# Performance work log

Measured on AMD Instinct MI355X. Metric: run time of the kernel, lower is better.

The kernel has to match this reference:

```python
import jax, jax.numpy as jnp
import numpy as np

# MoE_Bottleneck constants from source
E = 4   # number of experts
K = 2   # top-k routing


def setup_inputs() -> dict:
    key = jax.random.key(0)
    ks = jax.random.split(key, 10)
    B, C1, H, W = 8, 256, 64, 64
    C2 = 256
    Ch = C2 // 2  # c_ = int(c2*0.5) = 128
    x = jax.random.normal(ks[0], (B, C1, H, W), dtype=jnp.float32)
    # Conv = conv2d(no bias)+BN+SiLU; BN folded into weight scale + bias (eval mode).
    W1 = jax.random.normal(ks[1], (Ch, C1), dtype=jnp.float32) / np.sqrt(C1)
    b1 = jax.random.normal(ks[2], (Ch,), dtype=jnp.float32) * 0.1
    Wr = jax.random.normal(ks[3], (E, Ch), dtype=jnp.float32) / np.sqrt(Ch)
    br = jax.random.normal(ks[4], (E,), dtype=jnp.float32) * 0.1
    # Expert Conv(c_, c_, 3, 1): full 3x3 kernels [E, Cout, Cin, 3, 3]
    We = jax.random.normal(ks[5], (E, Ch, Ch, 3, 3), dtype=jnp.float32) / np.sqrt(Ch * 9)
    be = jax.random.normal(ks[6], (E, Ch), dtype=jnp.float32) * 0.1
    W3 = jax.random.normal(ks[7], (C2, Ch), dtype=jnp.float32) / np.sqrt(Ch)
    b3 = jax.random.normal(ks[8], (C2,), dtype=jnp.float32) * 0.1
    return {"x": x, "W1": W1, "b1": b1, "Wr": Wr, "br": br,
            "We": We, "be": be, "W3": W3, "b3": b3}


def reference(x, W1, b1, Wr, br, We, be, W3, b3):
    silu = jax.nn.silu
    # conv1: 1x1 conv + (folded BN) + SiLU
    x_in = silu(jnp.einsum('bchw,oc->bohw', x, W1) + b1[None, :, None, None])
    B, C, H, Wd = x_in.shape
    N = B * H * Wd
    xr = x_in.transpose(0, 2, 3, 1).reshape(N, C)            # [N, C] tokens
    # router: 1x1 conv -> per-pixel logits over E experts
    logits = xr @ Wr.T + br                                   # [N, E]
    probs = jax.nn.softmax(logits, axis=-1)
    topw, topi = jax.lax.top_k(probs, K)                      # [N, K]
    topw = topw / jnp.sum(topw, axis=-1, keepdims=True)       # renormalize top-k
    # dense [N, E] routing-weight matrix (indices within a row are unique)
    wmat = jnp.zeros_like(probs).at[jnp.arange(N)[:, None], topi].set(topw)
    # Experts: 3x3 conv applied to 1x1 spatial patches with pad=1 -> only the
    # center tap We[..., 1, 1] contributes (padding is zeros). Folded-BN bias + SiLU.
    Wc = We[:, :, :, 1, 1]                                    # [E, Cout, Cin]
    eout = silu(jnp.einsum('nc,eoc->neo', xr, Wc) + be[None]) # [N, E, C]
    moe = jnp.einsum('neo,ne->no', eout, wmat)                # weighted combine
    out = moe.reshape(B, H, Wd, C).transpose(0, 3, 1, 2)
    # conv3: 1x1 conv + SiLU
    y = silu(jnp.einsum('bchw,oc->bohw', out, W3) + b3[None, :, None, None])
    # shortcut=True and c1 == c2
    return y + x
```

## Files before the change

kernel.cpp:

```cpp
#include <hip/hip_runtime.h>
#include <hip/hip_bf16.h>


typedef unsigned short u16;
typedef unsigned int   u32;
typedef __attribute__((ext_vector_type(8))) short short8;
typedef __attribute__((ext_vector_type(4))) float f32x4;

#define MFMA16 __builtin_amdgcn_mfma_f32_16x16x32_bf16

__device__ __forceinline__ float silu_f(float v) { return v / (1.0f + __expf(-v)); }
__device__ __forceinline__ u16 f2bf(float f) {
    u32 u = __float_as_uint(f);
    return (u16)((u + 0x7fff + ((u >> 16) & 1)) >> 16);
}
__device__ __forceinline__ float bf2f(u16 h) { return __uint_as_float(((u32)h) << 16); }
__device__ __forceinline__ u32 pkbf(float a, float b) {
    __hip_bfloat162 h2 = __float22bfloat162_rn(make_float2(a, b));
    u32 r; __builtin_memcpy(&r, &h2, 4); return r;
}
__device__ __forceinline__ int swzkey(int row) { return (row ^ (row >> 2)) & 7; }

__global__ void prep_weights(const float* __restrict__ W1,
                             const float* __restrict__ We,
                             const float* __restrict__ W3,
                             u16* __restrict__ ws)
{
    int idx = blockIdx.x * 256 + threadIdx.x;
    if (idx < 36864) {
        int kc = idx / 9216, r = idx % 9216;
        int n = r / 72, j = r % 72;
        float v = (j < 64) ? W1[n * 256 + kc * 64 + j] : 0.0f;
        u16 h = f2bf(v);
        float lo = v - bf2f(h);
        ws[idx] = h;
        ws[36864 + idx] = f2bf(lo);
    } else if (idx < 102400) {
        int i = idx - 36864;
        int e = i >> 14, r = i & 16383;
        int o = r >> 7, rem = r & 127;
        int ps = rem >> 3, t = rem & 7;
        int gi = (ps & 8) | ((ps ^ swzkey(o)) & 7);
        int c = gi * 8 + t;
        ws[73728 + i] = f2bf(We[(size_t)(((e * 128 + o) * 128 + c) * 9) + 4]);
    } else if (idx < 135168) {
        int i = idx - 102400;
        int h = i >> 14, r = i & 16383;
        int o = r >> 7, rem = r & 127;
        int ps = rem >> 3, t = rem & 7;
        int gi = (ps & 8) | ((ps ^ swzkey(o)) & 7);
        int c = gi * 8 + t;
        ws[139264 + i] = f2bf(W3[(size_t)(h * 128 + o) * 128 + c]);
    }
}

__device__ __forceinline__ void stage_chunk(const u16* __restrict__ g, u16* l, int tid) {
#pragma unroll
    for (int i = 0; i < 8; ++i)
        __builtin_amdgcn_global_load_lds(g + (size_t)(i * 256 + tid) * 8,
                                         l + (size_t)(i * 256 + (tid & 192)) * 8, 16, 0, 0);
}
__device__ __forceinline__ void dma_u16(const u16* __restrict__ g, u16* l, int i, int tid) {
    int idx = i * 256 + tid;
    int ub  = i * 256 + (tid & 192);
    __builtin_amdgcn_global_load_lds(g + (size_t)idx * 8, l + ub * 8, 16, 0, 0);
}

__global__ __launch_bounds__(256, 2)
void fused_moe_mfma(const float* __restrict__ x,
                    const float* __restrict__ b1,
                    const float* __restrict__ Wrg,
                    const float* __restrict__ br,
                    const float* __restrict__ be,
                    const float* __restrict__ b3,
                    const u16* __restrict__ wbf,
                    float* __restrict__ out)
{
    __shared__ __align__(16) unsigned char smem[81920];
    u16*   const sWhi = (u16*)(smem);
    u16*   const sWlo = (u16*)(smem + 18432);
    u16*   const sAhi = (u16*)(smem + 36864);
    u16*   const sAlo = (u16*)(smem + 46080);
    u16*   const A2   = (u16*)(smem);
    u16*   const bufA = (u16*)(smem + 16384);
    u16*   const bufB = (u16*)(smem + 49152);
    float* const sY   = (float*)(smem + 16384);

    const int tid = threadIdx.x;
    const int l  = tid & 63;
    const int w  = tid >> 6;
    const int lr = l & 15;
    const int g  = l >> 4;
    const int lk = g * 8;
    const int mrow = 16 * w + 4 * g;
    const int arow = 16 * w + lr;
    const int akey = swzkey(arow);
    int okey[8];
#pragma unroll
    for (int f = 0; f < 8; ++f) okey[f] = swzkey(16 * f + lr);

    const int n0  = blockIdx.x << 6;
    const float* xb = x   + ((size_t)(n0 >> 12) * 256) * 4096 + (n0 & 4095);
    float*       ob = out + ((size_t)(n0 >> 12) * 256) * 4096 + (n0 & 4095);

    f32x4 acc1[8];
#pragma unroll
    for (int f = 0; f < 8; ++f) acc1[f] = (f32x4){0.f, 0.f, 0.f, 0.f};

    const int c2a = tid >> 4;
    const int c2b = 16 + c2a;
    const int m4  = (tid & 15) << 2;

#pragma unroll 1
    for (int kc = 0; kc < 4; ++kc) {
        __syncthreads();
        const float* xa0 = xb + (size_t)(kc * 64 + 2 * c2a) * 4096 + m4;
        const float* xa1 = xb + (size_t)(kc * 64 + 2 * c2b) * 4096 + m4;
        float4 fa0 = *(const float4*)xa0;
        float4 fb0 = *(const float4*)(xa0 + 4096);
        float4 fa1 = *(const float4*)xa1;
        float4 fb1 = *(const float4*)(xa1 + 4096);
#pragma unroll
        for (int i = 0; i < 5; ++i) {
            if (i * 256 + tid < 1152) {
                dma_u16(wbf + (size_t)kc * 9216,           sWhi, i, tid);
                dma_u16(wbf + (size_t)(36864 + kc * 9216), sWlo, i, tid);
            }
        }
        u32* H = (u32*)sAhi; u32* L = (u32*)sAlo;
        {
            float fav[4] = {fa0.x, fa0.y, fa0.z, fa0.w};
            float fbv[4] = {fb0.x, fb0.y, fb0.z, fb0.w};
#pragma unroll
            for (int r = 0; r < 4; ++r) {
                int ui = (m4 + r) * 36 + c2a;
                u32 hi = pkbf(fav[r], fbv[r]);
                float la = fav[r] - __uint_as_float(hi << 16);
                float lb = fbv[r] - __uint_as_float(hi & 0xffff0000u);
                H[ui] = hi; L[ui] = pkbf(la, lb);
            }
        }
        {
            float fav[4] = {fa1.x, fa1.y, fa1.z, fa1.w};
            float fbv[4] = {fb1.x, fb1.y, fb1.z, fb1.w};
#pragma unroll
            for (int r = 0; r < 4; ++r) {
                int ui = (m4 + r) * 36 + c2b;
                u32 hi = pkbf(fav[r], fbv[r]);
                float la = fav[r] - __uint_as_float(hi << 16);
                float lb = fbv[r] - __uint_as_float(hi & 0xffff0000u);
                H[ui] = hi; L[ui] = pkbf(la, lb);
            }
        }
        __syncthreads();
#pragma unroll
        for (int ks = 0; ks < 2; ++ks) {
            short8 ah = *(const short8*)&sAhi[(16 * w + lr) * 72 + ks * 32 + lk];
            short8 al = *(const short8*)&sAlo[(16 * w + lr) * 72 + ks * 32 + lk];
#pragma unroll
            for (int f = 0; f < 8; ++f) {
                int bo = (16 * f + lr) * 72 + ks * 32 + lk;
                short8 bh = *(const short8*)&sWhi[bo];
                short8 bl = *(const short8*)&sWlo[bo];
                acc1[f] = MFMA16(ah, bh, acc1[f], 0, 0, 0);
                acc1[f] = MFMA16(al, bh, acc1[f], 0, 0, 0);
                acc1[f] = MFMA16(ah, bl, acc1[f], 0, 0, 0);
                acc1[f] = MFMA16(al, bl, acc1[f], 0, 0, 0);
            }
        }
    }
    __syncthreads();

    stage_chunk(wbf + 73728,         bufA, tid);
    stage_chunk(wbf + 73728 + 16384, bufB, tid);

    float xin[8][4];
#pragma unroll
    for (int f = 0; f < 8; ++f) {
        float bias = b1[16 * f + lr];
#pragma unroll
        for (int i = 0; i < 4; ++i) xin[f][i] = silu_f(acc1[f][i] + bias);
    }
#pragma unroll
    for (int f = 0; f < 8; ++f) {
        int c = 16 * f + lr, gi = c >> 3;
#pragma unroll
        for (int i = 0; i < 4; ++i) {
            int m = mrow + i;
            int ps = (gi & 8) | ((gi ^ swzkey(m)) & 7);
            A2[m * 128 + ps * 8 + (c & 7)] = f2bf(xin[f][i]);
        }
    }

    float lg[4][4];
#pragma unroll
    for (int e = 0; e < 4; ++e)
#pragma unroll
        for (int i = 0; i < 4; ++i) lg[e][i] = 0.f;
#pragma unroll
    for (int f = 0; f < 8; ++f) {
        int c = 16 * f + lr;
        float w0 = Wrg[c], w1 = Wrg[128 + c], w2 = Wrg[256 + c], w3 = Wrg[384 + c];
#pragma unroll
        for (int i = 0; i < 4; ++i) {
            float xv = xin[f][i];
            lg[0][i] += xv * w0; lg[1][i] += xv * w1;
            lg[2][i] += xv * w2; lg[3][i] += xv * w3;
        }
    }
#pragma unroll
    for (int d = 1; d < 16; d <<= 1)
#pragma unroll
        for (int e = 0; e < 4; ++e)
#pragma unroll
            for (int i = 0; i < 4; ++i)
                lg[e][i] += __shfl_xor(lg[e][i], d, 64);

    float br0 = br[0], br1 = br[1], br2 = br[2], br3 = br[3];
    float rw[4][4];
#pragma unroll
    for (int i = 0; i < 4; ++i) {
        float le0 = lg[0][i] + br0, le1 = lg[1][i] + br1;
        float le2 = lg[2][i] + br2, le3 = lg[3][i] + br3;
        int c0 = (le1 > le0) + (le2 > le0) + (le3 > le0);
        int c1 = (le0 >= le1) + (le2 > le1) + (le3 > le1);
        int c2 = (le0 >= le2) + (le1 >= le2) + (le3 > le2);
        int c3 = (le0 >= le3) + (le1 >= le3) + (le2 >= le3);
        float m = fmaxf(fmaxf(le0, le1), fmaxf(le2, le3));
        float p0 = (c0 < 2) ? __expf(le0 - m) : 0.f;
        float p1 = (c1 < 2) ? __expf(le1 - m) : 0.f;
        float p2 = (c2 < 2) ? __expf(le2 - m) : 0.f;
        float p3 = (c3 < 2) ? __expf(le3 - m) : 0.f;
        float inv = 1.0f / (p0 + p1 + p2 + p3);
        rw[0][i] = p0 * inv; rw[1][i] = p1 * inv;
        rw[2][i] = p2 * inv; rw[3][i] = p3 * inv;
    }
    __syncthreads();

    f32x4 macc[8];
#pragma unroll
    for (int f = 0; f < 8; ++f) macc[f] = (f32x4){0.f, 0.f, 0.f, 0.f};

#pragma unroll 1
    for (int e = 0; e < 4; ++e) {
        const u16* Wb = (e & 1) ? bufB : bufA;
        f32x4 acce[8];
#pragma unroll
        for (int f = 0; f < 8; ++f) acce[f] = (f32x4){0.f, 0.f, 0.f, 0.f};
#pragma unroll
        for (int ks = 0; ks < 4; ++ks) {
            int gi = ks * 4 + g;
            int psA = (gi & 8) | ((gi ^ akey) & 7);
            short8 a = *(const short8*)&A2[arow * 128 + psA * 8];
#pragma unroll
            for (int f = 0; f < 8; ++f) {
                int psB = (gi & 8) | ((gi ^ okey[f]) & 7);
                short8 bb = *(const short8*)&Wb[(16 * f + lr) * 128 + psB * 8];
                acce[f] = MFMA16(a, bb, acce[f], 0, 0, 0);
            }
        }
#pragma unroll
        for (int f = 0; f < 8; ++f) {
            float bias = be[e * 128 + 16 * f + lr];
#pragma unroll
            for (int i = 0; i < 4; ++i)
                macc[f][i] += rw[e][i] * silu_f(acce[f][i] + bias);
        }
        __syncthreads();
        if (e < 2)      stage_chunk(wbf + 73728 + (e + 2) * 16384, (e & 1) ? bufB : bufA, tid);
        else if (e == 2) stage_chunk(wbf + 139264,                 bufA, tid);
        else              ;
    }

#pragma unroll
    for (int f = 0; f < 8; ++f) {
        int c = 16 * f + lr, gi = c >> 3;
#pragma unroll
        for (int i = 0; i < 4; ++i) {
            int m = mrow + i;
            int ps = (gi & 8) | ((gi ^ swzkey(m)) & 7);
            A2[m * 128 + ps * 8 + (c & 7)] = f2bf(macc[f][i]);
        }
    }
    __syncthreads();
    stage_chunk(wbf + 139264 + 16384, bufB, tid);

#pragma unroll 1
    for (int h = 0; h < 2; ++h) {
        const u16* Wb = h ? bufB : bufA;
        f32x4 acc3[8];
#pragma unroll
        for (int f = 0; f < 8; ++f) acc3[f] = (f32x4){0.f, 0.f, 0.f, 0.f};
#pragma unroll
        for (int ks = 0; ks < 4; ++ks) {
            int gi = ks * 4 + g;
            int psA = (gi & 8) | ((gi ^ akey) & 7);
            short8 a = *(const short8*)&A2[arow * 128 + psA * 8];
#pragma unroll
            for (int f = 0; f < 8; ++f) {
                int psB = (gi & 8) | ((gi ^ okey[f]) & 7);
                short8 bb = *(const short8*)&Wb[(16 * f + lr) * 128 + psB * 8];
                acc3[f] = MFMA16(a, bb, acc3[f], 0, 0, 0);
            }
        }
        __syncthreads();
        int mg = mrow >> 2;
#pragma unroll
        for (int f = 0; f < 8; ++f) {
            int o = 16 * f + lr;
            float bias = b3[h * 128 + o];
            float4 v;
            v.x = silu_f(acc3[f][0] + bias);
            v.y = silu_f(acc3[f][1] + bias);
            v.z = silu_f(acc3[f][2] + bias);
            v.w = silu_f(acc3[f][3] + bias);
            *(float4*)&sY[o * 64 + ((mg ^ okey[f]) << 2)] = v;
        }
        __syncthreads();
#pragma unroll
        for (int q = 0; q < 8; ++q) {
            int idx = q * 256 + tid;
            int o = idx >> 4, mq = idx & 15;
            int og = h * 128 + o;
            float4 vy = *(const float4*)&sY[o * 64 + ((mq ^ swzkey(o)) << 2)];
            size_t goff = (size_t)og * 4096 + (mq << 2);
            float4 r = *(const float4*)&xb[goff];
            vy.x += r.x; vy.y += r.y; vy.z += r.z; vy.w += r.w;
            *(float4*)&ob[goff] = vy;
        }
        if (h == 0) __syncthreads();
    }
}

extern "C" void kernel_launch(void* const* d_in, const int* in_sizes, int n_in,
                              void* d_out, int out_size, void* d_ws, size_t ws_size,
                              hipStream_t stream)
{
    const float* x  = (const float*)d_in[0];
    const float* W1 = (const float*)d_in[1];
    const float* b1 = (const float*)d_in[2];
    const float* Wr = (const float*)d_in[3];
    const float* br = (const float*)d_in[4];
    const float* We = (const float*)d_in[5];
    const float* be = (const float*)d_in[6];
    const float* W3 = (const float*)d_in[7];
    const float* b3 = (const float*)d_in[8];
    float* outp = (float*)d_out;
    u16* wbf = (u16*)d_ws;

    hipLaunchKernelGGL(prep_weights, dim3(528), dim3(256), 0, stream,
                       W1, We, W3, wbf);
    hipLaunchKernelGGL(fused_moe_mfma, dim3(512), dim3(256), 0, stream,
                       x, b1, Wr, br, be, b3, wbf, outp);
}
```

Before: 54.31 us.

## Split fused MoE kernel into three stage kernels with global intermediates

```diff
diff --git a/kernel.cpp b/kernel.cpp
--- a/kernel.cpp
+++ b/kernel.cpp
@@ -9,6 +9,13 @@
 
 #define MFMA16 __builtin_amdgcn_mfma_f32_16x16x32_bf16
 
+#define W1_OFF   0
+#define WE_OFF   65536
+#define W3_OFF   131072
+#define XIN_OFF  163840
+#define MOE_OFF  4358144
+#define RW_OFFU  8552448
+
 __device__ __forceinline__ float silu_f(float v) { return v / (1.0f + __expf(-v)); }
 __device__ __forceinline__ u16 f2bf(float f) {
     u32 u = __float_as_uint(f);
@@ -19,7 +26,8 @@
     __hip_bfloat162 h2 = __float22bfloat162_rn(make_float2(a, b));
     u32 r; __builtin_memcpy(&r, &h2, 4); return r;
 }
-__device__ __forceinline__ int swzkey(int row) { return (row ^ (row >> 2)) & 7; }
+__device__ __forceinline__ int key3(int r) { return (r ^ (r >> 2)) & 7; }
+__device__ __forceinline__ int key2(int r) { return (r ^ (r >> 2)) & 3; }
 
 __global__ void prep_weights(const float* __restrict__ W1,
                              const float* __restrict__ We,
@@ -27,141 +35,117 @@
                              u16* __restrict__ ws)
 {
     int idx = blockIdx.x * 256 + threadIdx.x;
-    if (idx < 36864) {
-        int kc = idx / 9216, r = idx % 9216;
-        int n = r / 72, j = r % 72;
-        float v = (j < 64) ? W1[n * 256 + kc * 64 + j] : 0.0f;
+    if (idx < 65536) {
+        int c4 = idx >> 14, r = idx & 16383;
+        int half = r >> 13, q = r & 8191;
+        int o = q >> 6, rem = q & 63;
+        int ps = rem >> 3, t = rem & 7;
+        int gi = (ps ^ key3(o)) & 7;
+        float v = W1[o * 256 + c4 * 64 + gi * 8 + t];
         u16 h = f2bf(v);
-        float lo = v - bf2f(h);
-        ws[idx] = h;
-        ws[36864 + idx] = f2bf(lo);
-    } else if (idx < 102400) {
-        int i = idx - 36864;
+        ws[idx] = half ? f2bf(v - bf2f(h)) : h;
+    } else if (idx < 131072) {
+        int i = idx - 65536;
         int e = i >> 14, r = i & 16383;
         int o = r >> 7, rem = r & 127;
         int ps = rem >> 3, t = rem & 7;
-        int gi = (ps & 8) | ((ps ^ swzkey(o)) & 7);
-        int c = gi * 8 + t;
-        ws[73728 + i] = f2bf(We[(size_t)(((e * 128 + o) * 128 + c) * 9) + 4]);
-    } else if (idx < 135168) {
-        int i = idx - 102400;
+        int gi = (ps & 8) | ((ps ^ key3(o)) & 7);
+        ws[idx] = f2bf(We[(size_t)(((e * 128 + o) * 128 + gi * 8 + t) * 9) + 4]);
+    } else if (idx < 163840) {
+        int i = idx - 131072;
         int h = i >> 14, r = i & 16383;
         int o = r >> 7, rem = r & 127;
         int ps = rem >> 3, t = rem & 7;
-        int gi = (ps & 8) | ((ps ^ swzkey(o)) & 7);
-        int c = gi * 8 + t;
-        ws[139264 + i] = f2bf(W3[(size_t)(h * 128 + o) * 128 + c]);
-    }
-}
-
-__device__ __forceinline__ void stage_chunk(const u16* __restrict__ g, u16* l, int tid) {
-#pragma unroll
-    for (int i = 0; i < 8; ++i)
-        __builtin_amdgcn_global_load_lds(g + (size_t)(i * 256 + tid) * 8,
-                                         l + (size_t)(i * 256 + (tid & 192)) * 8, 16, 0, 0);
-}
-__device__ __forceinline__ void dma_u16(const u16* __restrict__ g, u16* l, int i, int tid) {
-    int idx = i * 256 + tid;
-    int ub  = i * 256 + (tid & 192);
-    __builtin_amdgcn_global_load_lds(g + (size_t)idx * 8, l + ub * 8, 16, 0, 0);
-}
-
-__global__ __launch_bounds__(256, 2)
-void fused_moe_mfma(const float* __restrict__ x,
-                    const float* __restrict__ b1,
-                    const float* __restrict__ Wrg,
-                    const float* __restrict__ br,
-                    const float* __restrict__ be,
-                    const float* __restrict__ b3,
-                    const u16* __restrict__ wbf,
-                    float* __restrict__ out)
+        int gi = (ps & 8) | ((ps ^ key3(o)) & 7);
+        ws[131072 + i] = f2bf(W3[(size_t)(h * 128 + o) * 128 + gi * 8 + t]);
+    }
+}
+
+template<int ITER>
+__device__ __forceinline__ void stage512(const u16* __restrict__ g, u16* l, int tid) {
+#pragma unroll
+    for (int i = 0; i < ITER; ++i)
+        __builtin_amdgcn_global_load_lds(g + (size_t)(i * 512 + tid) * 8,
+                                         l + (size_t)(i * 512 + (tid & 448)) * 8, 16, 0, 0);
+}
+
+__global__ __launch_bounds__(512, 1)
+void k_gemm1(const float* __restrict__ x, const float* __restrict__ b1g,
+             const float* __restrict__ Wrg, const float* __restrict__ brg,
+             const u16* __restrict__ wbf, u16* __restrict__ xinG,
+             float* __restrict__ rwG)
 {
-    __shared__ __align__(16) unsigned char smem[81920];
-    u16*   const sWhi = (u16*)(smem);
-    u16*   const sWlo = (u16*)(smem + 18432);
-    u16*   const sAhi = (u16*)(smem + 36864);
-    u16*   const sAlo = (u16*)(smem + 46080);
-    u16*   const A2   = (u16*)(smem);
-    u16*   const bufA = (u16*)(smem + 16384);
-    u16*   const bufB = (u16*)(smem + 49152);
-    float* const sY   = (float*)(smem + 16384);
+    __shared__ __align__(16) u16 sm[49152];
+    u16* const wb0  = sm;
+    u16* const wb1  = sm + 16384;
+    u16* const ahi0 = sm + 32768;
+    u16* const alo0 = sm + 36864;
+    u16* const ahi1 = sm + 40960;
+    u16* const alo1 = sm + 45056;
 
     const int tid = threadIdx.x;
-    const int l  = tid & 63;
-    const int w  = tid >> 6;
-    const int lr = l & 15;
-    const int g  = l >> 4;
-    const int lk = g * 8;
+    const int l = tid & 63, w = tid >> 6;
+    const int lr = l & 15, g = l >> 4;
     const int mrow = 16 * w + 4 * g;
     const int arow = 16 * w + lr;
-    const int akey = swzkey(arow);
-    int okey[8];
-#pragma unroll
-    for (int f = 0; f < 8; ++f) okey[f] = swzkey(16 * f + lr);
-
-    const int n0  = blockIdx.x << 6;
-    const float* xb = x   + ((size_t)(n0 >> 12) * 256) * 4096 + (n0 & 4095);
-    float*       ob = out + ((size_t)(n0 >> 12) * 256) * 4096 + (n0 & 4095);
+    const int ak2 = key2(lr);
+    int ok3[8];
+#pragma unroll
+    for (int f = 0; f < 8; ++f) ok3[f] = key3(16 * f + lr);
+
+    const int n0 = blockIdx.x << 7;
+    const float* xb = x + ((size_t)(n0 >> 12) * 256) * 4096 + (n0 & 4095);
+
+    stage512<4>(wbf + W1_OFF, wb0, tid);
+
+    const int c2 = tid >> 5;
+    const int m4 = (tid & 31) << 2;
+    float4 fa = *(const float4*)&xb[(size_t)(2 * c2) * 4096 + m4];
+    float4 fb = *(const float4*)&xb[(size_t)(2 * c2 + 1) * 4096 + m4];
 
     f32x4 acc1[8];
 #pragma unroll
     for (int f = 0; f < 8; ++f) acc1[f] = (f32x4){0.f, 0.f, 0.f, 0.f};
 
-    const int c2a = tid >> 4;
-    const int c2b = 16 + c2a;
-    const int m4  = (tid & 15) << 2;
-
 #pragma unroll 1
-    for (int kc = 0; kc < 4; ++kc) {
-        __syncthreads();
-        const float* xa0 = xb + (size_t)(kc * 64 + 2 * c2a) * 4096 + m4;
-        const float* xa1 = xb + (size_t)(kc * 64 + 2 * c2b) * 4096 + m4;
-        float4 fa0 = *(const float4*)xa0;
-        float4 fb0 = *(const float4*)(xa0 + 4096);
-        float4 fa1 = *(const float4*)xa1;
-        float4 fb1 = *(const float4*)(xa1 + 4096);
-#pragma unroll
-        for (int i = 0; i < 5; ++i) {
-            if (i * 256 + tid < 1152) {
-                dma_u16(wbf + (size_t)kc * 9216,           sWhi, i, tid);
-                dma_u16(wbf + (size_t)(36864 + kc * 9216), sWlo, i, tid);
-            }
-        }
-        u32* H = (u32*)sAhi; u32* L = (u32*)sAlo;
+    for (int kc = 0; kc < 8; ++kc) {
         {
-            float fav[4] = {fa0.x, fa0.y, fa0.z, fa0.w};
-            float fbv[4] = {fb0.x, fb0.y, fb0.z, fb0.w};
+            u32* H = (u32*)((kc & 1) ? ahi1 : ahi0);
+            u32* L = (u32*)((kc & 1) ? alo1 : alo0);
+            float fav[4] = {fa.x, fa.y, fa.z, fa.w};
+            float fbv[4] = {fb.x, fb.y, fb.z, fb.w};
 #pragma unroll
             for (int r = 0; r < 4; ++r) {
-                int ui = (m4 + r) * 36 + c2a;
+                int row = m4 + r;
                 u32 hi = pkbf(fav[r], fbv[r]);
                 float la = fav[r] - __uint_as_float(hi << 16);
                 float lb = fbv[r] - __uint_as_float(hi & 0xffff0000u);
+                int ui = row * 16 + ((((c2 >> 2) ^ key2(row)) & 3) << 2) + (c2 & 3);
                 H[ui] = hi; L[ui] = pkbf(la, lb);
             }
         }
+        __syncthreads();
+        if (kc == 0 || kc == 2 || kc == 4) {
+            int c = kc / 2 + 1;
+            stage512<4>(wbf + W1_OFF + c * 16384, (c & 1) ? wb1 : wb0, tid);
+        }
+        if (kc < 7) {
+            fa = *(const float4*)&xb[(size_t)((kc + 1) * 32 + 2 * c2) * 4096 + m4];
+            fb = *(const float4*)&xb[(size_t)((kc + 1) * 32 + 2 * c2 + 1) * 4096 + m4];
+        }
         {
-            float fav[4] = {fa1.x, fa1.y, fa1.z, fa1.w};
-            float fbv[4] = {fb1.x, fb1.y, fb1.z, fb1.w};
-#pragma unroll
-            for (int r = 0; r < 4; ++r) {
-                int ui = (m4 + r) * 36 + c2b;
-                u32 hi = pkbf(fav[r], fbv[r]);
-                float la = fav[r] - __uint_as_float(hi << 16);
-                float lb = fbv[r] - __uint_as_float(hi & 0xffff0000u);
-                H[ui] = hi; L[ui] = pkbf(la, lb);
-            }
-        }
-        __syncthreads();
-#pragma unroll
-        for (int ks = 0; ks < 2; ++ks) {
-            short8 ah = *(const short8*)&sAhi[(16 * w + lr) * 72 + ks * 32 + lk];
-            short8 al = *(const short8*)&sAlo[(16 * w + lr) * 72 + ks * 32 + lk];
+            const u16* WB = ((kc >> 1) & 1) ? wb1 : wb0;
+            const u16* AH = (kc & 1) ? ahi1 : ahi0;
+            const u16* AL = (kc & 1) ? alo1 : alo0;
+            int aoff = arow * 32 + ((g ^ ak2) << 3);
+            short8 ah = *(const short8*)&AH[aoff];
+            short8 al = *(const short8*)&AL[aoff];
+            int gi = (kc & 1) * 4 + g;
 #pragma unroll
             for (int f = 0; f < 8; ++f) {
-                int bo = (16 * f + lr) * 72 + ks * 32 + lk;
-                short8 bh = *(const short8*)&sWhi[bo];
-                short8 bl = *(const short8*)&sWlo[bo];
+                int bo = (16 * f + lr) * 64 + (((gi ^ ok3[f]) & 7) << 3);
+                short8 bh = *(const short8*)&WB[bo];
+                short8 bl = *(const short8*)&WB[8192 + bo];
                 acc1[f] = MFMA16(ah, bh, acc1[f], 0, 0, 0);
                 acc1[f] = MFMA16(al, bh, acc1[f], 0, 0, 0);
                 acc1[f] = MFMA16(ah, bl, acc1[f], 0, 0, 0);
@@ -169,29 +153,24 @@
             }
         }
     }
-    __syncthreads();
-
-    stage_chunk(wbf + 73728,         bufA, tid);
-    stage_chunk(wbf + 73728 + 16384, bufB, tid);
 
     float xin[8][4];
 #pragma unroll
     for (int f = 0; f < 8; ++f) {
-        float bias = b1[16 * f + lr];
+        float bias = b1g[16 * f + lr];
 #pragma unroll
         for (int i = 0; i < 4; ++i) xin[f][i] = silu_f(acc1[f][i] + bias);
     }
 #pragma unroll
     for (int f = 0; f < 8; ++f) {
-        int c = 16 * f + lr, gi = c >> 3;
+        int c = 16 * f + lr, cg = c >> 3;
 #pragma unroll
         for (int i = 0; i < 4; ++i) {
             int m = mrow + i;
-            int ps = (gi & 8) | ((gi ^ swzkey(m)) & 7);
-            A2[m * 128 + ps * 8 + (c & 7)] = f2bf(xin[f][i]);
-        }
-    }
-
+            int ps = (cg & 8) | ((cg ^ key3(m)) & 7);
+            xinG[(size_t)(n0 + m) * 128 + ps * 8 + (c & 7)] = f2bf(xin[f][i]);
+        }
+    }
     float lg[4][4];
 #pragma unroll
     for (int e = 0; e < 4; ++e)
@@ -216,114 +195,178 @@
             for (int i = 0; i < 4; ++i)
                 lg[e][i] += __shfl_xor(lg[e][i], d, 64);
 
-    float br0 = br[0], br1 = br[1], br2 = br[2], br3 = br[3];
-    float rw[4][4];
+    float br0 = brg[0], br1 = brg[1], br2 = brg[2], br3 = brg[3];
+    if (lr == 0) {
+#pragma unroll
+        for (int i = 0; i < 4; ++i) {
+            float le0 = lg[0][i] + br0, le1 = lg[1][i] + br1;
+            float le2 = lg[2][i] + br2, le3 = lg[3][i] + br3;
+            int c0 = (le1 > le0) + (le2 > le0) + (le3 > le0);
+            int c1 = (le0 >= le1) + (le2 > le1) + (le3 > le1);
+            int c2r = (le0 >= le2) + (le1 >= le2) + (le3 > le2);
+            int c3 = (le0 >= le3) + (le1 >= le3) + (le2 >= le3);
+            float m = fmaxf(fmaxf(le0, le1), fmaxf(le2, le3));
+            float p0 = (c0 < 2) ? __expf(le0 - m) : 0.f;
+            float p1 = (c1 < 2) ? __expf(le1 - m) : 0.f;
+            float p2 = (c2r < 2) ? __expf(le2 - m) : 0.f;
+            float p3 = (c3 < 2) ? __expf(le3 - m) : 0.f;
+            float inv = 1.0f / (p0 + p1 + p2 + p3);
+            float4 v; v.x = p0 * inv; v.y = p1 * inv; v.z = p2 * inv; v.w = p3 * inv;
+            *(float4*)&rwG[(size_t)(n0 + mrow + i) * 4] = v;
+        }
+    }
+}
+
+__global__ __launch_bounds__(512, 1)
+void k_experts(const float* __restrict__ beg, const u16* __restrict__ wbf,
+               const u16* __restrict__ xinG, const float* __restrict__ rwG,
+               u16* __restrict__ moeG)
+{
+    __shared__ __align__(16) u16 sm[49152];
+    u16* const eb0 = sm;
+    u16* const eb1 = sm + 16384;
+    u16* const xt  = sm + 32768;
+
+    const int tid = threadIdx.x;
+    const int l = tid & 63, w = tid >> 6;
+    const int lr = l & 15, g = l >> 4;
+    const int mrow = 16 * w + 4 * g;
+    const int arow = 16 * w + lr;
+    const int ak3 = key3(arow);
+    int ok3[8];
+#pragma unroll
+    for (int f = 0; f < 8; ++f) ok3[f] = key3(16 * f + lr);
+
+    const int n0 = blockIdx.x << 7;
+
+    stage512<4>(wbf + WE_OFF, eb0, tid);
+    stage512<4>(wbf + WE_OFF + 16384, eb1, tid);
+    stage512<4>(xinG + (size_t)n0 * 128, xt, tid);
+
+    float rwa[4][4];
 #pragma unroll
     for (int i = 0; i < 4; ++i) {
-        float le0 = lg[0][i] + br0, le1 = lg[1][i] + br1;
-        float le2 = lg[2][i] + br2, le3 = lg[3][i] + br3;
-        int c0 = (le1 > le0) + (le2 > le0) + (le3 > le0);
-        int c1 = (le0 >= le1) + (le2 > le1) + (le3 > le1);
-        int c2 = (le0 >= le2) + (le1 >= le2) + (le3 > le2);
-        int c3 = (le0 >= le3) + (le1 >= le3) + (le2 >= le3);
-        float m = fmaxf(fmaxf(le0, le1), fmaxf(le2, le3));
-        float p0 = (c0 < 2) ? __expf(le0 - m) : 0.f;
-        float p1 = (c1 < 2) ? __expf(le1 - m) : 0.f;
-        float p2 = (c2 < 2) ? __expf(le2 - m) : 0.f;
-        float p3 = (c3 < 2) ? __expf(le3 - m) : 0.f;
-        float inv = 1.0f / (p0 + p1 + p2 + p3);
-        rw[0][i] = p0 * inv; rw[1][i] = p1 * inv;
-        rw[2][i] = p2 * inv; rw[3][i] = p3 * inv;
-    }
+        float4 v = *(const float4*)&rwG[(size_t)(n0 + mrow + i) * 4];
+        rwa[0][i] = v.x; rwa[1][i] = v.y; rwa[2][i] = v.z; rwa[3][i] = v.w;
+    }
+    float bev[4][8];
+#pragma unroll
+    for (int e = 0; e < 4; ++e)
+#pragma unroll
+        for (int f = 0; f < 8; ++f) bev[e][f] = beg[e * 128 + 16 * f + lr];
+
+    f32x4 macc[8];
+#pragma unroll
+    for (int f = 0; f < 8; ++f) macc[f] = (f32x4){0.f, 0.f, 0.f, 0.f};
+
     __syncthreads();
-
-    f32x4 macc[8];
-#pragma unroll
-    for (int f = 0; f < 8; ++f) macc[f] = (f32x4){0.f, 0.f, 0.f, 0.f};
 
 #pragma unroll 1
     for (int e = 0; e < 4; ++e) {
-        const u16* Wb = (e & 1) ? bufB : bufA;
+        const u16* Wb = (e & 1) ? eb1 : eb0;
         f32x4 acce[8];
 #pragma unroll
         for (int f = 0; f < 8; ++f) acce[f] = (f32x4){0.f, 0.f, 0.f, 0.f};
 #pragma unroll
         for (int ks = 0; ks < 4; ++ks) {
             int gi = ks * 4 + g;
-            int psA = (gi & 8) | ((gi ^ akey) & 7);
-            short8 a = *(const short8*)&A2[arow * 128 + psA * 8];
+            int psA = (gi & 8) | ((gi ^ ak3) & 7);
+            short8 a = *(const short8*)&xt[arow * 128 + psA * 8];
 #pragma unroll
             for (int f = 0; f < 8; ++f) {
-                int psB = (gi & 8) | ((gi ^ okey[f]) & 7);
+                int psB = (gi & 8) | ((gi ^ ok3[f]) & 7);
                 short8 bb = *(const short8*)&Wb[(16 * f + lr) * 128 + psB * 8];
                 acce[f] = MFMA16(a, bb, acce[f], 0, 0, 0);
             }
         }
 #pragma unroll
-        for (int f = 0; f < 8; ++f) {
-            float bias = be[e * 128 + 16 * f + lr];
+        for (int f = 0; f < 8; ++f)
 #pragma unroll
             for (int i = 0; i < 4; ++i)
-                macc[f][i] += rw[e][i] * silu_f(acce[f][i] + bias);
-        }
+                macc[f][i] += rwa[e][i] * silu_f(acce[f][i] + bev[e][f]);
         __syncthreads();
-        if (e < 2)      stage_chunk(wbf + 73728 + (e + 2) * 16384, (e & 1) ? bufB : bufA, tid);
-        else if (e == 2) stage_chunk(wbf + 139264,                 bufA, tid);
-        else              ;
-    }
-
+        if (e < 2) stage512<4>(wbf + WE_OFF + (e + 2) * 16384, (e & 1) ? eb1 : eb0, tid);
+    }
 #pragma unroll
     for (int f = 0; f < 8; ++f) {
-        int c = 16 * f + lr, gi = c >> 3;
+        int c = 16 * f + lr, cg = c >> 3;
 #pragma unroll
         for (int i = 0; i < 4; ++i) {
             int m = mrow + i;
-            int ps = (gi & 8) | ((gi ^ swzkey(m)) & 7);
-            A2[m * 128 + ps * 8 + (c & 7)] = f2bf(macc[f][i]);
-        }
-    }
+            int ps = (cg & 8) | ((cg ^ key3(m)) & 7);
+            moeG[(size_t)(n0 + m) * 128 + ps * 8 + (c & 7)] = f2bf(macc[f][i]);
+        }
+    }
+}
+
+__global__ __launch_bounds__(512, 1)
+void k_gemm3(const float* __restrict__ x, const float* __restrict__ b3g,
+             const u16* __restrict__ wbf, const u16* __restrict__ moeG,
+             float* __restrict__ out)
+{
+    __shared__ __align__(16) u16 sm[65536];
+    u16*   const w3s = sm;
+    u16*   const mt  = sm + 16384;
+    float* const sY  = (float*)(sm + 32768);
+
+    const int tid = threadIdx.x;
+    const int l = tid & 63, w = tid >> 6;
+    const int lr = l & 15, g = l >> 4;
+    const int mrow = 16 * w + 4 * g;
+    const int arow = 16 * w + lr;
+    const int ak3 = key3(arow);
+    int ok3[8];
+#pragma unroll
+    for (int f = 0; f < 8; ++f) ok3[f] = key3(16 * f + lr);
+
+    const int n0 = blockIdx.x << 7;
+    const float* xb = x   + ((size_t)(n0 >> 12) * 256) * 4096 + (n0 & 4095);
+    float*       ob = out + ((size_t)(n0 >> 12) * 256) * 4096 + (n0 & 4095);
+
+    stage512<4>(wbf + W3_OFF, w3s, tid);
+    stage512<4>(moeG + (size_t)n0 * 128, mt, tid);
     __syncthreads();
-    stage_chunk(wbf + 139264 + 16384, bufB, tid);
 
 #pragma unroll 1
     for (int h = 0; h < 2; ++h) {
-        const u16* Wb = h ? bufB : bufA;
         f32x4 acc3[8];
 #pragma unroll
         for (int f = 0; f < 8; ++f) acc3[f] = (f32x4){0.f, 0.f, 0.f, 0.f};
 #pragma unroll
         for (int ks = 0; ks < 4; ++ks) {
             int gi = ks * 4 + g;
-            int psA = (gi & 8) | ((gi ^ akey) & 7);
-            short8 a = *(const short8*)&A2[arow * 128 + psA * 8];
+            int psA = (gi & 8) | ((gi ^ ak3) & 7);
+            short8 a = *(const short8*)&mt[arow * 128 + psA * 8];
 #pragma unroll
             for (int f = 0; f < 8; ++f) {
-                int psB = (gi & 8) | ((gi ^ okey[f]) & 7);
-                short8 bb = *(const short8*)&Wb[(16 * f + lr) * 128 + psB * 8];
+                int psB = (gi & 8) | ((gi ^ ok3[f]) & 7);
+                short8 bb = *(const short8*)&w3s[(16 * f + lr) * 128 + psB * 8];
                 acc3[f] = MFMA16(a, bb, acc3[f], 0, 0, 0);
             }
         }
         __syncthreads();
+        if (h == 0) stage512<4>(wbf + W3_OFF + 16384, w3s, tid);
         int mg = mrow >> 2;
 #pragma unroll
         for (int f = 0; f < 8; ++f) {
-            int o = 16 * f + lr;
-            float bias = b3[h * 128 + o];
+            int c = 16 * f + lr;
+            float bias = b3g[h * 128 + c];
             float4 v;
             v.x = silu_f(acc3[f][0] + bias);
             v.y = silu_f(acc3[f][1] + bias);
             v.z = silu_f(acc3[f][2] + bias);
             v.w = silu_f(acc3[f][3] + bias);
-            *(float4*)&sY[o * 64 + ((mg ^ okey[f]) << 2)] = v;
+            int ps = (mg & 24) | ((mg ^ key3(c)) & 7);
+            *(float4*)&sY[c * 128 + ps * 4] = v;
         }
         __syncthreads();
 #pragma unroll
         for (int q = 0; q < 8; ++q) {
-            int idx = q * 256 + tid;
-            int o = idx >> 4, mq = idx & 15;
-            int og = h * 128 + o;
-            float4 vy = *(const float4*)&sY[o * 64 + ((mq ^ swzkey(o)) << 2)];
-            size_t goff = (size_t)og * 4096 + (mq << 2);
+            int idx = q * 512 + tid;
+            int c = idx >> 5, mq = idx & 31;
+            int ps = (mq & 24) | ((mq ^ key3(c)) & 7);
+            float4 vy = *(const float4*)&sY[c * 128 + ps * 4];
+            size_t goff = (size_t)(h * 128 + c) * 4096 + (mq << 2);
             float4 r = *(const float4*)&xb[goff];
             vy.x += r.x; vy.y += r.y; vy.z += r.z; vy.w += r.w;
             *(float4*)&ob[goff] = vy;
@@ -346,10 +389,18 @@
     const float* W3 = (const float*)d_in[7];
     const float* b3 = (const float*)d_in[8];
     float* outp = (float*)d_out;
-    u16* wbf = (u16*)d_ws;
-
-    hipLaunchKernelGGL(prep_weights, dim3(528), dim3(256), 0, stream,
+
+    u16*   wbf  = (u16*)d_ws;
+    u16*   xinG = wbf + XIN_OFF;
+    u16*   moeG = wbf + MOE_OFF;
+    float* rwG  = (float*)(wbf + RW_OFFU);
+
+    hipLaunchKernelGGL(prep_weights, dim3(640), dim3(256), 0, stream,
                        W1, We, W3, wbf);
-    hipLaunchKernelGGL(fused_moe_mfma, dim3(512), dim3(256), 0, stream,
-                       x, b1, Wr, br, be, b3, wbf, outp);
-}
+    hipLaunchKernelGGL(k_gemm1, dim3(256), dim3(512), 0, stream,
+                       x, b1, Wr, br, wbf, xinG, rwG);
+    hipLaunchKernelGGL(k_experts, dim3(256), dim3(512), 0, stream,
+                       be, wbf, xinG, rwG, moeG);
+    hipLaunchKernelGGL(k_gemm3, dim3(256), dim3(512), 0, stream,
+                       x, b3, wbf, moeG, outp);
+}
```

Measured after the change: 64.14 us. 18.1% more time.

## Split output channels across 8 waves per block with cross-wave router reduction

Applied to the files above, without the earlier changes.

```diff
diff --git a/kernel.cpp b/kernel.cpp
--- a/kernel.cpp
+++ b/kernel.cpp
@@ -19,7 +19,7 @@
     __hip_bfloat162 h2 = __float22bfloat162_rn(make_float2(a, b));
     u32 r; __builtin_memcpy(&r, &h2, 4); return r;
 }
-__device__ __forceinline__ int swzkey(int row) { return (row ^ (row >> 2)) & 7; }
+__device__ __forceinline__ int key3(int r) { return (r ^ (r >> 2)) & 7; }
 
 __global__ void prep_weights(const float* __restrict__ W1,
                              const float* __restrict__ We,
@@ -40,7 +40,7 @@
         int e = i >> 14, r = i & 16383;
         int o = r >> 7, rem = r & 127;
         int ps = rem >> 3, t = rem & 7;
-        int gi = (ps & 8) | ((ps ^ swzkey(o)) & 7);
+        int gi = (ps & 8) | ((ps ^ key3(o)) & 7);
         int c = gi * 8 + t;
         ws[73728 + i] = f2bf(We[(size_t)(((e * 128 + o) * 128 + c) * 9) + 4]);
     } else if (idx < 135168) {
@@ -48,7 +48,7 @@
         int h = i >> 14, r = i & 16383;
         int o = r >> 7, rem = r & 127;
         int ps = rem >> 3, t = rem & 7;
-        int gi = (ps & 8) | ((ps ^ swzkey(o)) & 7);
+        int gi = (ps & 8) | ((ps ^ key3(o)) & 7);
         int c = gi * 8 + t;
         ws[139264 + i] = f2bf(W3[(size_t)(h * 128 + o) * 128 + c]);
     }
@@ -56,23 +56,18 @@
 
 __device__ __forceinline__ void stage_chunk(const u16* __restrict__ g, u16* l, int tid) {
 #pragma unroll
-    for (int i = 0; i < 8; ++i)
-        __builtin_amdgcn_global_load_lds(g + (size_t)(i * 256 + tid) * 8,
-                                         l + (size_t)(i * 256 + (tid & 192)) * 8, 16, 0, 0);
-}
-__device__ __forceinline__ void dma_u16(const u16* __restrict__ g, u16* l, int i, int tid) {
-    int idx = i * 256 + tid;
-    int ub  = i * 256 + (tid & 192);
-    __builtin_amdgcn_global_load_lds(g + (size_t)idx * 8, l + ub * 8, 16, 0, 0);
-}
-
-__global__ __launch_bounds__(256, 2)
+    for (int i = 0; i < 4; ++i)
+        __builtin_amdgcn_global_load_lds(g + (size_t)(i * 512 + tid) * 8,
+                                         l + (size_t)(i * 512 + (tid & 448)) * 8, 16, 0, 0);
+}
+
+__global__ __launch_bounds__(512, 4)
 void fused_moe_mfma(const float* __restrict__ x,
-                    const float* __restrict__ b1,
+                    const float* __restrict__ b1g,
                     const float* __restrict__ Wrg,
-                    const float* __restrict__ br,
-                    const float* __restrict__ be,
-                    const float* __restrict__ b3,
+                    const float* __restrict__ brg,
+                    const float* __restrict__ beg,
+                    const float* __restrict__ b3g,
                     const u16* __restrict__ wbf,
                     float* __restrict__ out)
 {
@@ -84,82 +79,73 @@
     u16*   const A2   = (u16*)(smem);
     u16*   const bufA = (u16*)(smem + 16384);
     u16*   const bufB = (u16*)(smem + 49152);
+    float* const sLg  = (float*)(smem + 49152);
     float* const sY   = (float*)(smem + 16384);
 
     const int tid = threadIdx.x;
     const int l  = tid & 63;
     const int w  = tid >> 6;
+    const int wm = w & 3, wn = w >> 2;
     const int lr = l & 15;
     const int g  = l >> 4;
-    const int lk = g * 8;
-    const int mrow = 16 * w + 4 * g;
-    const int arow = 16 * w + lr;
-    const int akey = swzkey(arow);
-    int okey[8];
-#pragma unroll
-    for (int f = 0; f < 8; ++f) okey[f] = swzkey(16 * f + lr);
+    const int mrow = 16 * wm + 4 * g;
+    const int arow = 16 * wm + lr;
+    const int ak3 = key3(arow);
+    int oc[4], ok3[4];
+#pragma unroll
+    for (int f = 0; f < 4; ++f) { oc[f] = 64 * wn + 16 * f + lr; ok3[f] = key3(oc[f]); }
 
     const int n0  = blockIdx.x << 6;
     const float* xb = x   + ((size_t)(n0 >> 12) * 256) * 4096 + (n0 & 4095);
     float*       ob = out + ((size_t)(n0 >> 12) * 256) * 4096 + (n0 & 4095);
 
-    f32x4 acc1[8];
-#pragma unroll
-    for (int f = 0; f < 8; ++f) acc1[f] = (f32x4){0.f, 0.f, 0.f, 0.f};
-
-    const int c2a = tid >> 4;
-    const int c2b = 16 + c2a;
-    const int m4  = (tid & 15) << 2;
+    f32x4 acc1[4];
+#pragma unroll
+    for (int f = 0; f < 4; ++f) acc1[f] = (f32x4){0.f, 0.f, 0.f, 0.f};
+
+    const int c2 = tid >> 4;
+    const int m4 = (tid & 15) << 2;
 
 #pragma unroll 1
     for (int kc = 0; kc < 4; ++kc) {
         __syncthreads();
-        const float* xa0 = xb + (size_t)(kc * 64 + 2 * c2a) * 4096 + m4;
-        const float* xa1 = xb + (size_t)(kc * 64 + 2 * c2b) * 4096 + m4;
-        float4 fa0 = *(const float4*)xa0;
-        float4 fb0 = *(const float4*)(xa0 + 4096);
-        float4 fa1 = *(const float4*)xa1;
-        float4 fb1 = *(const float4*)(xa1 + 4096);
-#pragma unroll
-        for (int i = 0; i < 5; ++i) {
-            if (i * 256 + tid < 1152) {
-                dma_u16(wbf + (size_t)kc * 9216,           sWhi, i, tid);
-                dma_u16(wbf + (size_t)(36864 + kc * 9216), sWlo, i, tid);
-            }
-        }
-        u32* H = (u32*)sAhi; u32* L = (u32*)sAlo;
+        const float* xa = xb + (size_t)(kc * 64 + 2 * c2) * 4096 + m4;
+        float4 fa = *(const float4*)xa;
+        float4 fb = *(const float4*)(xa + 4096);
+#pragma unroll
+        for (int i = 0; i < 3; ++i) {
+            int idx = i * 512 + tid;
+            if (idx < 1152) {
+                int ub = i * 512 + (tid & 448);
+                __builtin_amdgcn_global_load_lds(wbf + (size_t)kc * 9216 + (size_t)idx * 8,
+                                                 sWhi + (size_t)ub * 8, 16, 0, 0);
+                __builtin_amdgcn_global_load_lds(wbf + (size_t)(36864 + kc * 9216) + (size_t)idx * 8,
+                                                 sWlo + (size_t)ub * 8, 16, 0, 0);
+            }
+        }
         {
-            float fav[4] = {fa0.x, fa0.y, fa0.z, fa0.w};
-            float fbv[4] = {fb0.x, fb0.y, fb0.z, fb0.w};
+            u32* H = (u32*)sAhi; u32* L = (u32*)sAlo;
+            float fav[4] = {fa.x, fa.y, fa.z, fa.w};
+            float fbv[4] = {fb.x, fb.y, fb.z, fb.w};
 #pragma unroll
             for (int r = 0; r < 4; ++r) {
-                int ui = (m4 + r) * 36 + c2a;
+                int row = m4 + r;
                 u32 hi = pkbf(fav[r], fbv[r]);
                 float la = fav[r] - __uint_as_float(hi << 16);
                 float lb = fbv[r] - __uint_as_float(hi & 0xffff0000u);
-                H[ui] = hi; L[ui] = pkbf(la, lb);
-            }
-        }
-        {
-            float fav[4] = {fa1.x, fa1.y, fa1.z, fa1.w};
-            float fbv[4] = {fb1.x, fb1.y, fb1.z, fb1.w};
-#pragma unroll
-            for (int r = 0; r < 4; ++r) {
-                int ui = (m4 + r) * 36 + c2b;
-                u32 hi = pkbf(fav[r], fbv[r]);
-                float la = fav[r] - __uint_as_float(hi << 16);
-                float lb = fbv[r] - __uint_as_float(hi & 0xffff0000u);
-                H[ui] = hi; L[ui] = pkbf(la, lb);
+                int jj = c2 ^ (key3(row) << 2);
+                H[row * 36 + jj] = hi; L[row * 36 + jj] = pkbf(la, lb);
             }
         }
         __syncthreads();
 #pragma unroll
         for (int ks = 0; ks < 2; ++ks) {
-            short8 ah = *(const short8*)&sAhi[(16 * w + lr) * 72 + ks * 32 + lk];
-            short8 al = *(const short8*)&sAlo[(16 * w + lr) * 72 + ks * 32 + lk];
-#pragma unroll
-            for (int f = 0; f < 8; ++f) {
-                int bo = (16 * f + lr) * 72 + ks * 32 + lk;
+            int jb = (ks * 16 + g * 4) ^ (ak3 << 2);
+            short8 ah = *(const short8*)&sAhi[arow * 72 + jb * 2];
+            short8 al = *(const short8*)&sAlo[arow * 72 + jb * 2];
+#pragma unroll
+            for (int f = 0; f < 4; ++f) {
+                int bo = oc[f] * 72 + ks * 32 + g * 8;
                 short8 bh = *(const short8*)&sWhi[bo];
                 short8 bl = *(const short8*)&sWlo[bo];
                 acc1[f] = MFMA16(ah, bh, acc1[f], 0, 0, 0);
@@ -170,36 +156,33 @@
         }
     }
     __syncthreads();
-
-    stage_chunk(wbf + 73728,         bufA, tid);
-    stage_chunk(wbf + 73728 + 16384, bufB, tid);
-
-    float xin[8][4];
-#pragma unroll
-    for (int f = 0; f < 8; ++f) {
-        float bias = b1[16 * f + lr];
+    stage_chunk(wbf + 73728, bufA, tid);
+
+    float xin[4][4];
+#pragma unroll
+    for (int f = 0; f < 4; ++f) {
+        float bias = b1g[oc[f]];
 #pragma unroll
         for (int i = 0; i < 4; ++i) xin[f][i] = silu_f(acc1[f][i] + bias);
     }
 #pragma unroll
-    for (int f = 0; f < 8; ++f) {
-        int c = 16 * f + lr, gi = c >> 3;
+    for (int f = 0; f < 4; ++f) {
+        int c = oc[f], cg = c >> 3;
 #pragma unroll
         for (int i = 0; i < 4; ++i) {
             int m = mrow + i;
-            int ps = (gi & 8) | ((gi ^ swzkey(m)) & 7);
+            int ps = (cg & 8) | ((cg ^ key3(m)) & 7);
             A2[m * 128 + ps * 8 + (c & 7)] = f2bf(xin[f][i]);
         }
     }
-
     float lg[4][4];
 #pragma unroll
     for (int e = 0; e < 4; ++e)
 #pragma unroll
         for (int i = 0; i < 4; ++i) lg[e][i] = 0.f;
 #pragma unroll
-    for (int f = 0; f < 8; ++f) {
-        int c = 16 * f + lr;
+    for (int f = 0; f < 4; ++f) {
+        int c = oc[f];
         float w0 = Wrg[c], w1 = Wrg[128 + c], w2 = Wrg[256 + c], w3 = Wrg[384 + c];
 #pragma unroll
         for (int i = 0; i < 4; ++i) {
@@ -215,70 +198,81 @@
 #pragma unroll
             for (int i = 0; i < 4; ++i)
                 lg[e][i] += __shfl_xor(lg[e][i], d, 64);
-
-    float br0 = br[0], br1 = br[1], br2 = br[2], br3 = br[3];
+    if (lr == 0) {
+#pragma unroll
+        for (int i = 0; i < 4; ++i)
+#pragma unroll
+            for (int e = 0; e < 4; ++e)
+                sLg[(wn * 64 + mrow + i) * 4 + e] = lg[e][i];
+    }
+    __syncthreads();
+
+    float br0 = brg[0], br1 = brg[1], br2 = brg[2], br3 = brg[3];
     float rw[4][4];
 #pragma unroll
     for (int i = 0; i < 4; ++i) {
-        float le0 = lg[0][i] + br0, le1 = lg[1][i] + br1;
-        float le2 = lg[2][i] + br2, le3 = lg[3][i] + br3;
+        int m = mrow + i;
+        float le0 = sLg[m * 4 + 0] + sLg[(64 + m) * 4 + 0] + br0;
+        float le1 = sLg[m * 4 + 1] + sLg[(64 + m) * 4 + 1] + br1;
+        float le2 = sLg[m * 4 + 2] + sLg[(64 + m) * 4 + 2] + br2;
+        float le3 = sLg[m * 4 + 3] + sLg[(64 + m) * 4 + 3] + br3;
         int c0 = (le1 > le0) + (le2 > le0) + (le3 > le0);
         int c1 = (le0 >= le1) + (le2 > le1) + (le3 > le1);
-        int c2 = (le0 >= le2) + (le1 >= le2) + (le3 > le2);
+        int c2r = (le0 >= le2) + (le1 >= le2) + (le3 > le2);
         int c3 = (le0 >= le3) + (le1 >= le3) + (le2 >= le3);
-        float m = fmaxf(fmaxf(le0, le1), fmaxf(le2, le3));
-        float p0 = (c0 < 2) ? __expf(le0 - m) : 0.f;
-        float p1 = (c1 < 2) ? __expf(le1 - m) : 0.f;
-        float p2 = (c2 < 2) ? __expf(le2 - m) : 0.f;
-        float p3 = (c3 < 2) ? __expf(le3 - m) : 0.f;
+        float m0 = fmaxf(fmaxf(le0, le1), fmaxf(le2, le3));
+        float p0 = (c0 < 2) ? __expf(le0 - m0) : 0.f;
+        float p1 = (c1 < 2) ? __expf(le1 - m0) : 0.f;
+        float p2 = (c2r < 2) ? __expf(le2 - m0) : 0.f;
+        float p3 = (c3 < 2) ? __expf(le3 - m0) : 0.f;
         float inv = 1.0f / (p0 + p1 + p2 + p3);
         rw[0][i] = p0 * inv; rw[1][i] = p1 * inv;
         rw[2][i] = p2 * inv; rw[3][i] = p3 * inv;
     }
     __syncthreads();
-
-    f32x4 macc[8];
-#pragma unroll
-    for (int f = 0; f < 8; ++f) macc[f] = (f32x4){0.f, 0.f, 0.f, 0.f};
+    stage_chunk(wbf + 73728 + 16384, bufB, tid);
+
+    f32x4 macc[4];
+#pragma unroll
+    for (int f = 0; f < 4; ++f) macc[f] = (f32x4){0.f, 0.f, 0.f, 0.f};
 
 #pragma unroll 1
     for (int e = 0; e < 4; ++e) {
         const u16* Wb = (e & 1) ? bufB : bufA;
-        f32x4 acce[8];
-#pragma unroll
-        for (int f = 0; f < 8; ++f) acce[f] = (f32x4){0.f, 0.f, 0.f, 0.f};
+        f32x4 acce[4];
+#pragma unroll
+        for (int f = 0; f < 4; ++f) acce[f] = (f32x4){0.f, 0.f, 0.f, 0.f};
 #pragma unroll
         for (int ks = 0; ks < 4; ++ks) {
             int gi = ks * 4 + g;
-            int psA = (gi & 8) | ((gi ^ akey) & 7);
+            int psA = (gi & 8) | ((gi ^ ak3) & 7);
             short8 a = *(const short8*)&A2[arow * 128 + psA * 8];
 #pragma unroll
-            for (int f = 0; f < 8; ++f) {
-                int psB = (gi & 8) | ((gi ^ okey[f]) & 7);
-                short8 bb = *(const short8*)&Wb[(16 * f + lr) * 128 + psB * 8];
+            for (int f = 0; f < 4; ++f) {
+                int psB = (gi & 8) | ((gi ^ ok3[f]) & 7);
+                short8 bb = *(const short8*)&Wb[oc[f] * 128 + psB * 8];
                 acce[f] = MFMA16(a, bb, acce[f], 0, 0, 0);
             }
         }
 #pragma unroll
-        for (int f = 0; f < 8; ++f) {
-            float bias = be[e * 128 + 16 * f + lr];
+        for (int f = 0; f < 4; ++f) {
+            float bias = beg[e * 128 + oc[f]];
 #pragma unroll
             for (int i = 0; i < 4; ++i)
                 macc[f][i] += rw[e][i] * silu_f(acce[f][i] + bias);
         }
         __syncthreads();
-        if (e < 2)      stage_chunk(wbf + 73728 + (e + 2) * 16384, (e & 1) ? bufB : bufA, tid);
-        else if (e == 2) stage_chunk(wbf + 139264,                 bufA, tid);
-        else              ;
-    }
-
-#pragma unroll
-    for (int f = 0; f < 8; ++f) {
-        int c = 16 * f + lr, gi = c >> 3;
+        if (e < 2)       stage_chunk(wbf + 73728 + (e + 2) * 16384, (e & 1) ? bufB : bufA, tid);
+        else if (e == 2) stage_chunk(wbf + 139264, bufA, tid);
+    }
+
+#pragma unroll
+    for (int f = 0; f < 4; ++f) {
+        int c = oc[f], cg = c >> 3;
 #pragma unroll
         for (int i = 0; i < 4; ++i) {
             int m = mrow + i;
-            int ps = (gi & 8) | ((gi ^ swzkey(m)) & 7);
+            int ps = (cg & 8) | ((cg ^ key3(m)) & 7);
             A2[m * 128 + ps * 8 + (c & 7)] = f2bf(macc[f][i]);
         }
     }
@@ -288,41 +282,41 @@
 #pragma unroll 1
     for (int h = 0; h < 2; ++h) {
         const u16* Wb = h ? bufB : bufA;
-        f32x4 acc3[8];
-#pragma unroll
-        for (int f = 0; f < 8; ++f) acc3[f] = (f32x4){0.f, 0.f, 0.f, 0.f};
+        f32x4 acc3[4];
+#pragma unroll
+        for (int f = 0; f < 4; ++f) acc3[f] = (f32x4){0.f, 0.f, 0.f, 0.f};
 #pragma unroll
         for (int ks = 0; ks < 4; ++ks) {
             int gi = ks * 4 + g;
-            int psA = (gi & 8) | ((gi ^ akey) & 7);
+            int psA = (gi & 8) | ((gi ^ ak3) & 7);
             short8 a = *(const short8*)&A2[arow * 128 + psA * 8];
 #pragma unroll
-            for (int f = 0; f < 8; ++f) {
-                int psB = (gi & 8) | ((gi ^ okey[f]) & 7);
-                short8 bb = *(const short8*)&Wb[(16 * f + lr) * 128 + psB * 8];
+            for (int f = 0; f < 4; ++f) {
+                int psB = (gi & 8) | ((gi ^ ok3[f]) & 7);
+                short8 bb = *(const short8*)&Wb[oc[f] * 128 + psB * 8];
                 acc3[f] = MFMA16(a, bb, acc3[f], 0, 0, 0);
             }
         }
         __syncthreads();
         int mg = mrow >> 2;
 #pragma unroll
-        for (int f = 0; f < 8; ++f) {
-            int o = 16 * f + lr;
-            float bias = b3[h * 128 + o];
+        for (int f = 0; f < 4; ++f) {
+            int o = oc[f];
+            float bias = b3g[h * 128 + o];
             float4 v;
             v.x = silu_f(acc3[f][0] + bias);
             v.y = silu_f(acc3[f][1] + bias);
             v.z = silu_f(acc3[f][2] + bias);
             v.w = silu_f(acc3[f][3] + bias);
-            *(float4*)&sY[o * 64 + ((mg ^ okey[f]) << 2)] = v;
-        }
-        __syncthreads();
-#pragma unroll
-        for (int q = 0; q < 8; ++q) {
-            int idx = q * 256 + tid;
+            *(float4*)&sY[o * 64 + ((mg ^ ok3[f]) << 2)] = v;
+        }
+        __syncthreads();
+#pragma unroll
+        for (int q = 0; q < 4; ++q) {
+            int idx = q * 512 + tid;
             int o = idx >> 4, mq = idx & 15;
             int og = h * 128 + o;
-            float4 vy = *(const float4*)&sY[o * 64 + ((mq ^ swzkey(o)) << 2)];
+            float4 vy = *(const float4*)&sY[o * 64 + ((mq ^ key3(o)) << 2)];
             size_t goff = (size_t)og * 4096 + (mq << 2);
             float4 r = *(const float4*)&xb[goff];
             vy.x += r.x; vy.y += r.y; vy.z += r.z; vy.w += r.w;
@@ -350,6 +344,6 @@
 
     hipLaunchKernelGGL(prep_weights, dim3(528), dim3(256), 0, stream,
                        W1, We, W3, wbf);
-    hipLaunchKernelGGL(fused_moe_mfma, dim3(512), dim3(256), 0, stream,
+    hipLaunchKernelGGL(fused_moe_mfma, dim3(512), dim3(512), 0, stream,
                        x, b1, Wr, br, be, b3, wbf, outp);
 }
```

New measurement: 51.11 us. 1.06x faster.
